# Kernel tuning notes

Hardware: AMD Instinct MI355X
Metric: run time of the kernel (lower is better)

## Reference

```python
import jax, jax.numpy as jnp
import numpy as np

S = 1024      # seq_len (capped by module's precomputed rows/cols tables)
B = 8         # batch
E = 512       # embed_dim
PD = 192      # pos_dim
H = 8         # num_heads
QHD = 32      # query_head_dim (== key_head_dim)
PHD = 4       # pos_head_dim
IN_DIM = (2 * QHD + PHD) * H  # 544


def setup_inputs() -> dict:
    key = jax.random.key(0)
    k0, k1, k2, k3 = jax.random.split(key, 4)
    x = jax.random.normal(k0, (S, B, E), jnp.float32)
    pos_emb = jax.random.normal(k1, (B, 2 * S - 1, PD), jnp.float32)
    # ScaledLinear(embed_dim, in_proj_dim, initial_scale=query_head_dim**-0.25)
    W_in = jax.random.normal(k2, (E, IN_DIM), jnp.float32) * (QHD ** -0.25) / np.sqrt(E).astype(np.float32)
    b_in = jnp.zeros((IN_DIM,), jnp.float32)
    # ScaledLinear(pos_dim, num_heads*pos_head_dim, bias=False, initial_scale=0.05)
    W_pos = jax.random.normal(k3, (PD, H * PHD), jnp.float32) * (0.05 / np.sqrt(PD).astype(np.float32))
    return {"x": x, "pos_emb": pos_emb, "W_in": W_in, "b_in": b_in, "W_pos": W_pos}


def reference(x, pos_emb, W_in, b_in, W_pos):
    s, b, _ = x.shape
    h, qhd, phd = H, QHD, PHD
    qdim = h * qhd

    proj = x @ W_in + b_in                      # [S, B, 544]
    q = proj[..., :qdim].reshape(s, b, h, qhd)          # [S,B,H,Dq]
    k = proj[..., qdim:2 * qdim].reshape(s, b, h, qhd)  # [S,B,H,Dq]
    p = proj[..., 2 * qdim:].reshape(s, b, h, phd)      # [S,B,H,Dp]

    # attn_scores[h,b,i,j] = q_i . k_j
    attn_scores = jnp.einsum('sbhd,tbhd->hbst', q, k)   # [H,B,S,S]

    # positional projection: [B, 2S-1, H, Dp]
    pe = (pos_emb @ W_pos).reshape(b, 2 * s - 1, h, phd)
    pos_scores = jnp.einsum('sbhd,bnhd->hbsn', p, pe)   # [H,B,S,2S-1]

    # relative skew: index[i,j] = (S-1-i) + j  (matches rows[-S:]+cols gather)
    idx = (s - 1) - jnp.arange(s)[:, None] + jnp.arange(s)[None, :]  # [S,S]
    idx_b = jnp.broadcast_to(idx[None, None], (h, b, s, s))
    rel = jnp.take_along_axis(pos_scores, idx_b, axis=-1)            # [H,B,S,S]

    return jax.nn.softmax(attn_scores + rel, axis=-1)
```

## Files before the change

### kernel.cpp

```cpp
#include <hip/hip_runtime.h>
#include <hip/hip_fp16.h>

#define S_LEN 1024
#define BATCH 8
#define EMB 512
#define POSD 192
#define NH 8
#define QHD 32
#define PHD 4
#define IN_DIM 544
#define QDIM 256
#define NPOS 2047

typedef _Float16 half8 __attribute__((ext_vector_type(8)));
typedef _Float16 half4_t __attribute__((ext_vector_type(4)));
typedef _Float16 half2_t __attribute__((ext_vector_type(2)));
typedef float f32x4 __attribute__((ext_vector_type(4)));

static __device__ __forceinline__ float fdot2(half2_t a, half2_t b, float c) {
#if __has_builtin(__builtin_amdgcn_fdot2)
  return __builtin_amdgcn_fdot2(a, b, c, false);
#else
  return c + (float)a[0] * (float)b[0] + (float)a[1] * (float)b[1];
#endif
}

__global__ __launch_bounds__(256) void wconv_kernel(const float* __restrict__ W_in,
                                                    const float* __restrict__ W_pos,
                                                    _Float16* __restrict__ Wt,
                                                    _Float16* __restrict__ WtP) {
  const int blk = blockIdx.x;
  const int tid = threadIdx.x;
  if (blk < 72) {
    __shared__ float T[64][65];
    const int bx = blk % 9;
    const int by = blk / 9;
    const int n0 = bx * 64, e0 = by * 64;
    const int r = tid >> 4, c4 = (tid & 15) * 4;
    if (n0 + c4 < IN_DIM) {
      #pragma unroll
      for (int rr = 0; rr < 64; rr += 16) {
        f32x4 v = *(const f32x4*)(W_in + (size_t)(e0 + r + rr) * IN_DIM + n0 + c4);
        T[r + rr][c4] = v[0]; T[r + rr][c4 + 1] = v[1];
        T[r + rr][c4 + 2] = v[2]; T[r + rr][c4 + 3] = v[3];
      }
    }
    __syncthreads();
    const int nl = tid >> 2, ec = (tid & 3) * 16;
    const int n = n0 + nl;
    if (n < IN_DIM) {
      half8 h0, h1;
      #pragma unroll
      for (int j = 0; j < 8; ++j) {
        h0[j] = (_Float16)T[ec + j][nl];
        h1[j] = (_Float16)T[ec + 8 + j][nl];
      }
      *(half8*)(Wt + (size_t)n * EMB + e0 + ec) = h0;
      *(half8*)(Wt + (size_t)n * EMB + e0 + ec + 8) = h1;
    }
  } else {
    for (int i = tid; i < 32 * POSD; i += 256) {
      int c = i / POSD, k = i % POSD;
      WtP[i] = (_Float16)W_pos[(size_t)k * 32 + c];
    }
  }
}

__global__ __launch_bounds__(256) void pe_kernel(const float* __restrict__ pos_emb,
                                                 const _Float16* __restrict__ WtP,
                                                 _Float16* __restrict__ pe16) {
  __shared__ __align__(16) _Float16 As[64][200];
  const int b = blockIdx.y, chunk = blockIdx.x;
  const int n0 = chunk * 64;
  const int tid = threadIdx.x;
  const int row = tid >> 2, sc = tid & 3;
  const bool rowok = (n0 + row) < NPOS;
  const float* src = pos_emb + ((size_t)b * NPOS + n0 + row) * POSD + sc * 48;
  #pragma unroll
  for (int j = 0; j < 6; ++j) {
    f32x4 v0 = {}, v1 = {};
    if (rowok) { v0 = *(const f32x4*)(src + j * 8); v1 = *(const f32x4*)(src + j * 8 + 4); }
    half8 h;
    #pragma unroll
    for (int t = 0; t < 4; ++t) { h[t] = (_Float16)v0[t]; h[4 + t] = (_Float16)v1[t]; }
    *(half8*)&As[row][sc * 48 + j * 8] = h;
  }
  __syncthreads();
  const int w = tid >> 6, l = tid & 63, g = l >> 4, lg = l & 15;
  f32x4 acc0 = {}, acc1 = {};
  f32x4* accp[2] = {&acc0, &acc1};
  #pragma unroll
  for (int kk = 0; kk < POSD; kk += 32) {
    half8 aF = *(const half8*)&As[w * 16 + lg][kk + g * 8];
    half8 b0 = *(const half8*)(WtP + (size_t)lg * POSD + kk + g * 8);
    half8 b1 = *(const half8*)(WtP + (size_t)(16 + lg) * POSD + kk + g * 8);
    acc0 = __builtin_amdgcn_mfma_f32_16x16x32_f16(aF, b0, acc0, 0, 0, 0);
    acc1 = __builtin_amdgcn_mfma_f32_16x16x32_f16(aF, b1, acc1, 0, 0, 0);
  }
  #pragma unroll
  for (int t = 0; t < 2; ++t) {
    int c = t * 16 + lg, h = c >> 2, d = c & 3;
    _Float16* dst = pe16 + ((size_t)(b * NH + h) * NPOS) * PHD + d;
    f32x4 a = *accp[t];
    #pragma unroll
    for (int r = 0; r < 4; ++r) {
      int n = n0 + w * 16 + 4 * g + r;
      if (n < NPOS) dst[(size_t)n * PHD] = (_Float16)a[r];
    }
  }
}

__global__ __launch_bounds__(256) void proj_kernel(const float* __restrict__ x,
                                                   const _Float16* __restrict__ Wt,
                                                   const float* __restrict__ bias,
                                                   _Float16* __restrict__ q16,
                                                   _Float16* __restrict__ k16,
                                                   _Float16* __restrict__ p16) {
  __shared__ __align__(16) _Float16 As[64][40];
  __shared__ __align__(16) _Float16 Bs[64][40];
  const int m0 = blockIdx.x * 64;
  const int n0 = blockIdx.y * 64;
  const int tid = threadIdx.x;
  const int w = tid >> 6, l = tid & 63, g = l >> 4, lg = l & 15;
  const int wm = w >> 1, wn = w & 1;
  const int srow = tid >> 2, sc = tid & 3;

  f32x4 acc[2][2] = {};

  for (int k0 = 0; k0 < EMB; k0 += 32) {
    const float* asrc = x + (size_t)(m0 + srow) * EMB + k0 + sc * 8;
    f32x4 a0 = *(const f32x4*)asrc;
    f32x4 a1 = *(const f32x4*)(asrc + 4);
    half8 ah;
    #pragma unroll
    for (int j = 0; j < 4; ++j) { ah[j] = (_Float16)a0[j]; ah[4 + j] = (_Float16)a1[j]; }
    int nrow = n0 + srow;
    half8 bh8 = {};
    if (nrow < IN_DIM) bh8 = *(const half8*)(Wt + (size_t)nrow * EMB + k0 + sc * 8);
    *(half8*)&As[srow][sc * 8] = ah;
    *(half8*)&Bs[srow][sc * 8] = bh8;
    __syncthreads();
    half8 aF0 = *(const half8*)&As[wm * 32 + lg][g * 8];
    half8 aF1 = *(const half8*)&As[wm * 32 + 16 + lg][g * 8];
    half8 bF0 = *(const half8*)&Bs[wn * 32 + lg][g * 8];
    half8 bF1 = *(const half8*)&Bs[wn * 32 + 16 + lg][g * 8];
    acc[0][0] = __builtin_amdgcn_mfma_f32_16x16x32_f16(aF0, bF0, acc[0][0], 0, 0, 0);
    acc[0][1] = __builtin_amdgcn_mfma_f32_16x16x32_f16(aF0, bF1, acc[0][1], 0, 0, 0);
    acc[1][0] = __builtin_amdgcn_mfma_f32_16x16x32_f16(aF1, bF0, acc[1][0], 0, 0, 0);
    acc[1][1] = __builtin_amdgcn_mfma_f32_16x16x32_f16(aF1, bF1, acc[1][1], 0, 0, 0);
    __syncthreads();
  }

  #pragma unroll
  for (int sm = 0; sm < 2; ++sm)
    #pragma unroll
    for (int sn = 0; sn < 2; ++sn)
      #pragma unroll
      for (int r = 0; r < 4; ++r) {
        int m = m0 + wm * 32 + sm * 16 + 4 * g + r;
        int n = n0 + wn * 32 + sn * 16 + lg;
        if (n < IN_DIM) {
          float v = acc[sm][sn][r] + bias[n];
          _Float16 hv = (_Float16)v;
          int s = m >> 3, b = m & 7;
          if (n < QDIM) {
            int h = n >> 5, d = n & 31;
            q16[(((size_t)(b * NH + h)) * S_LEN + s) * QHD + d] = hv;
          } else if (n < 2 * QDIM) {
            int n2 = n - QDIM;
            int h = n2 >> 5, d = n2 & 31;
            k16[(((size_t)(b * NH + h)) * S_LEN + s) * QHD + d] = hv;
          } else {
            int n2 = n - 2 * QDIM;
            int h = n2 >> 2, d = n2 & 3;
            p16[(((size_t)(b * NH + h)) * S_LEN + s) * PHD + d] = hv;
          }
        }
      }
}

__global__ __launch_bounds__(256, 4) void attn_kernel(const _Float16* __restrict__ q16,
                                                      const _Float16* __restrict__ k16,
                                                      const _Float16* __restrict__ p16,
                                                      const _Float16* __restrict__ pe16,
                                                      float* __restrict__ out) {
  __shared__ __align__(16) _Float16 peLDS[1040 * 4];
  __shared__ float wred[4][16];
  __shared__ __align__(16) float sbuf[4][16][68];
  const int bid = blockIdx.x;
  const int swz = (bid & 7) * 512 + (bid >> 3);
  const int bh = swz >> 6;
  const int rblk = swz & 63;
  const int b = bh >> 3, h = bh & 7;
  const int i0 = rblk * 16;
  const int tid = threadIdx.x;
  const int w = tid >> 6, l = tid & 63, g = l >> 4, lg = l & 15;
  const int nlo = S_LEN - 16 - i0;

  for (int it = tid; it < 1039; it += 256) {
    *(uint2*)&peLDS[it * 4] =
        *(const uint2*)&pe16[((size_t)bh * NPOS + nlo + it) * 4];
  }

  const _Float16* qbase = q16 + ((size_t)bh * S_LEN + i0) * QHD;
  half8 qF = *(const half8*)(qbase + lg * QHD + g * 8);

  const _Float16* pbase = p16 + ((size_t)bh * S_LEN + i0 + lg) * PHD;
  half2_t pq0 = *(const half2_t*)(pbase);
  half2_t pq1 = *(const half2_t*)(pbase + 2);

  __syncthreads();

  const _Float16* kbase = k16 + (size_t)bh * S_LEN * QHD;
  const int jw = w * 256;
  f32x4 zero = {};
  float s = 0.f;
  half4_t probs[16];

  #pragma unroll
  for (int ct = 0; ct < 16; ++ct) {
    int j = jw + ct * 16 + lg;
    half8 kF = *(const half8*)(kbase + (size_t)j * QHD + g * 8);
    f32x4 a = __builtin_amdgcn_mfma_f32_16x16x32_f16(kF, qF, zero, 0, 0, 0);
    int nl0 = 15 - lg + jw + ct * 16 + 4 * g;
    half4_t ph;
    #pragma unroll
    for (int r = 0; r < 4; ++r) {
      half4_t pv4 = *(const half4_t*)&peLDS[(nl0 + r) * 4];
      half2_t lo = {pv4[0], pv4[1]};
      half2_t hi = {pv4[2], pv4[3]};
      float sc = fdot2(pq1, hi, fdot2(pq0, lo, a[r]));
      float e = __expf(sc - 6.0f);
      s += e;
      ph[r] = (_Float16)e;
    }
    probs[ct] = ph;
  }

  s += __shfl_xor(s, 16);
  s += __shfl_xor(s, 32);
  if (g == 0) wred[w][lg] = s;
  __syncthreads();
  s = (wred[0][lg] + wred[1][lg]) + (wred[2][lg] + wred[3][lg]);
  const float inv = 1.0f / s;

  const size_t orow0 = ((size_t)(h * BATCH + b) * S_LEN + i0) * S_LEN;
  #pragma unroll
  for (int chunk = 0; chunk < 4; ++chunk) {
    #pragma unroll
    for (int cc = 0; cc < 4; ++cc) {
      half4_t ph = probs[chunk * 4 + cc];
      f32x4 v;
      #pragma unroll
      for (int r = 0; r < 4; ++r) v[r] = (float)ph[r] * inv;
      *(f32x4*)&sbuf[w][lg][cc * 16 + 4 * g] = v;
    }
    asm volatile("s_waitcnt lgkmcnt(0)" ::: "memory");
    __builtin_amdgcn_sched_barrier(0);
    #pragma unroll
    for (int k2 = 0; k2 < 4; ++k2) {
      int rr = k2 * 4 + g;
      f32x4 v = *(const f32x4*)&sbuf[w][rr][lg * 4];
      *(f32x4*)(out + orow0 + (size_t)rr * S_LEN + jw + chunk * 64 + lg * 4) = v;
    }
    asm volatile("s_waitcnt lgkmcnt(0)" ::: "memory");
    __builtin_amdgcn_sched_barrier(0);
  }
}

extern "C" void kernel_launch(void* const* d_in, const int* in_sizes, int n_in,
                              void* d_out, int out_size, void* d_ws, size_t ws_size,
                              hipStream_t stream) {
  const float* x = (const float*)d_in[0];
  const float* pos_emb = (const float*)d_in[1];
  const float* W_in = (const float*)d_in[2];
  const float* b_in = (const float*)d_in[3];
  const float* W_pos = (const float*)d_in[4];
  float* out = (float*)d_out;

  char* ws = (char*)d_ws;
  _Float16* Wt = (_Float16*)(ws);
  _Float16* q16 = (_Float16*)(ws + 557056);
  _Float16* k16 = (_Float16*)(ws + 557056 + 4194304);
  _Float16* p16 = (_Float16*)(ws + 557056 + 2 * 4194304);
  _Float16* pe16 = (_Float16*)(ws + 557056 + 2 * 4194304 + 524288);
  _Float16* WtP = p16;

  wconv_kernel<<<dim3(73), dim3(256), 0, stream>>>(W_in, W_pos, Wt, WtP);
  pe_kernel<<<dim3(32, BATCH), dim3(256), 0, stream>>>(pos_emb, WtP, pe16);
  proj_kernel<<<dim3(128, 9), dim3(256), 0, stream>>>(x, Wt, b_in, q16, k16, p16);
  attn_kernel<<<dim3(4096), dim3(256), 0, stream>>>(q16, k16, p16, pe16, out);
}
```

Measured before the change: 91.32 us.

## Merge weight conversion with pos-embedding projection and retile input projection GEMM

Folds the W_pos conversion and the positional projection into one prep kernel. Each block converts W_pos into shared memory itself, so one kernel launch and the global staging buffer go away. The projection GEMM moves to 128x64 tiles with a 64-wide K step, staging fp32 x tiles in swizzled shared memory and converting to fp16 at fragment load. This means fewer barriers and K iterations, at the cost of larger shared memory use and redundant W_pos work in every pe block.

```diff
diff --git a/kernel.cpp b/kernel.cpp
--- a/kernel.cpp
+++ b/kernel.cpp
@@ -25,14 +25,16 @@
 #endif
 }
 
-__global__ __launch_bounds__(256) void wconv_kernel(const float* __restrict__ W_in,
-                                                    const float* __restrict__ W_pos,
-                                                    _Float16* __restrict__ Wt,
-                                                    _Float16* __restrict__ WtP) {
+__global__ __launch_bounds__(256) void prep_kernel(const float* __restrict__ W_in,
+                                                   const float* __restrict__ W_pos,
+                                                   const float* __restrict__ pos_emb,
+                                                   _Float16* __restrict__ Wt,
+                                                   _Float16* __restrict__ pe16) {
+  __shared__ __align__(16) char smem[38400];
   const int blk = blockIdx.x;
   const int tid = threadIdx.x;
   if (blk < 72) {
-    __shared__ float T[64][65];
+    float (*T)[65] = reinterpret_cast<float(*)[65]>(smem);
     const int bx = blk % 9;
     const int by = blk / 9;
     const int n0 = bx * 64, e0 = by * 64;
@@ -59,53 +61,52 @@
       *(half8*)(Wt + (size_t)n * EMB + e0 + ec + 8) = h1;
     }
   } else {
-    for (int i = tid; i < 32 * POSD; i += 256) {
-      int c = i / POSD, k = i % POSD;
-      WtP[i] = (_Float16)W_pos[(size_t)k * 32 + c];
-    }
-  }
-}
-
-__global__ __launch_bounds__(256) void pe_kernel(const float* __restrict__ pos_emb,
-                                                 const _Float16* __restrict__ WtP,
-                                                 _Float16* __restrict__ pe16) {
-  __shared__ __align__(16) _Float16 As[64][200];
-  const int b = blockIdx.y, chunk = blockIdx.x;
-  const int n0 = chunk * 64;
-  const int tid = threadIdx.x;
-  const int row = tid >> 2, sc = tid & 3;
-  const bool rowok = (n0 + row) < NPOS;
-  const float* src = pos_emb + ((size_t)b * NPOS + n0 + row) * POSD + sc * 48;
-  #pragma unroll
-  for (int j = 0; j < 6; ++j) {
-    f32x4 v0 = {}, v1 = {};
-    if (rowok) { v0 = *(const f32x4*)(src + j * 8); v1 = *(const f32x4*)(src + j * 8 + 4); }
-    half8 h;
-    #pragma unroll
-    for (int t = 0; t < 4; ++t) { h[t] = (_Float16)v0[t]; h[4 + t] = (_Float16)v1[t]; }
-    *(half8*)&As[row][sc * 48 + j * 8] = h;
-  }
-  __syncthreads();
-  const int w = tid >> 6, l = tid & 63, g = l >> 4, lg = l & 15;
-  f32x4 acc0 = {}, acc1 = {};
-  f32x4* accp[2] = {&acc0, &acc1};
-  #pragma unroll
-  for (int kk = 0; kk < POSD; kk += 32) {
-    half8 aF = *(const half8*)&As[w * 16 + lg][kk + g * 8];
-    half8 b0 = *(const half8*)(WtP + (size_t)lg * POSD + kk + g * 8);
-    half8 b1 = *(const half8*)(WtP + (size_t)(16 + lg) * POSD + kk + g * 8);
-    acc0 = __builtin_amdgcn_mfma_f32_16x16x32_f16(aF, b0, acc0, 0, 0, 0);
-    acc1 = __builtin_amdgcn_mfma_f32_16x16x32_f16(aF, b1, acc1, 0, 0, 0);
-  }
-  #pragma unroll
-  for (int t = 0; t < 2; ++t) {
-    int c = t * 16 + lg, h = c >> 2, d = c & 3;
-    _Float16* dst = pe16 + ((size_t)(b * NH + h) * NPOS) * PHD + d;
-    f32x4 a = *accp[t];
-    #pragma unroll
-    for (int r = 0; r < 4; ++r) {
-      int n = n0 + w * 16 + 4 * g + r;
-      if (n < NPOS) dst[(size_t)n * PHD] = (_Float16)a[r];
+    _Float16 (*As)[200] = reinterpret_cast<_Float16(*)[200]>(smem);
+    _Float16 (*Wl)[200] = reinterpret_cast<_Float16(*)[200]>(smem + 25600);
+    const int id = blk - 72;
+    const int chunk = id & 31, b = id >> 5;
+    const int n0 = chunk * 64;
+    #pragma unroll
+    for (int p = 0; p < 6; ++p) {
+      int f = (p * 256 + tid) * 4;
+      f32x4 v = *(const f32x4*)(W_pos + f);
+      int k = f >> 5, c = f & 31;
+      #pragma unroll
+      for (int t = 0; t < 4; ++t) Wl[c + t][k] = (_Float16)v[t];
+    }
+    const int row = tid >> 2, sc = tid & 3;
+    const bool rowok = (n0 + row) < NPOS;
+    const float* src = pos_emb + ((size_t)b * NPOS + n0 + row) * POSD + sc * 48;
+    #pragma unroll
+    for (int j = 0; j < 6; ++j) {
+      f32x4 v0 = {}, v1 = {};
+      if (rowok) { v0 = *(const f32x4*)(src + j * 8); v1 = *(const f32x4*)(src + j * 8 + 4); }
+      half8 h;
+      #pragma unroll
+      for (int t = 0; t < 4; ++t) { h[t] = (_Float16)v0[t]; h[4 + t] = (_Float16)v1[t]; }
+      *(half8*)&As[row][sc * 48 + j * 8] = h;
+    }
+    __syncthreads();
+    const int w = tid >> 6, l = tid & 63, g = l >> 4, lg = l & 15;
+    f32x4 acc0 = {}, acc1 = {};
+    #pragma unroll
+    for (int kk = 0; kk < POSD; kk += 32) {
+      half8 aF = *(const half8*)&As[w * 16 + lg][kk + g * 8];
+      half8 b0 = *(const half8*)&Wl[lg][kk + g * 8];
+      half8 b1 = *(const half8*)&Wl[16 + lg][kk + g * 8];
+      acc0 = __builtin_amdgcn_mfma_f32_16x16x32_f16(aF, b0, acc0, 0, 0, 0);
+      acc1 = __builtin_amdgcn_mfma_f32_16x16x32_f16(aF, b1, acc1, 0, 0, 0);
+    }
+    f32x4 accs[2] = {acc0, acc1};
+    #pragma unroll
+    for (int t = 0; t < 2; ++t) {
+      int c = t * 16 + lg, h = c >> 2, d = c & 3;
+      _Float16* dst = pe16 + ((size_t)(b * NH + h) * NPOS) * PHD + d;
+      #pragma unroll
+      for (int r2 = 0; r2 < 4; ++r2) {
+        int n = n0 + w * 16 + 4 * g + r2;
+        if (n < NPOS) dst[(size_t)n * PHD] = (_Float16)accs[t][r2];
+      }
     }
   }
 }
@@ -116,51 +117,73 @@
                                                    _Float16* __restrict__ q16,
                                                    _Float16* __restrict__ k16,
                                                    _Float16* __restrict__ p16) {
-  __shared__ __align__(16) _Float16 As[64][40];
-  __shared__ __align__(16) _Float16 Bs[64][40];
-  const int m0 = blockIdx.x * 64;
+  __shared__ __align__(16) float At[128 * 64];
+  __shared__ __align__(16) _Float16 Bt[64 * 64];
+  const int m0 = blockIdx.x * 128;
   const int n0 = blockIdx.y * 64;
   const int tid = threadIdx.x;
   const int w = tid >> 6, l = tid & 63, g = l >> 4, lg = l & 15;
   const int wm = w >> 1, wn = w & 1;
-  const int srow = tid >> 2, sc = tid & 3;
-
-  f32x4 acc[2][2] = {};
-
-  for (int k0 = 0; k0 < EMB; k0 += 32) {
-    const float* asrc = x + (size_t)(m0 + srow) * EMB + k0 + sc * 8;
-    f32x4 a0 = *(const f32x4*)asrc;
-    f32x4 a1 = *(const f32x4*)(asrc + 4);
-    half8 ah;
-    #pragma unroll
-    for (int j = 0; j < 4; ++j) { ah[j] = (_Float16)a0[j]; ah[4 + j] = (_Float16)a1[j]; }
-    int nrow = n0 + srow;
-    half8 bh8 = {};
-    if (nrow < IN_DIM) bh8 = *(const half8*)(Wt + (size_t)nrow * EMB + k0 + sc * 8);
-    *(half8*)&As[srow][sc * 8] = ah;
-    *(half8*)&Bs[srow][sc * 8] = bh8;
+
+  f32x4 acc[4][2] = {};
+
+  for (int ks = 0; ks < 8; ++ks) {
+    const int k0 = ks * 64;
     __syncthreads();
-    half8 aF0 = *(const half8*)&As[wm * 32 + lg][g * 8];
-    half8 aF1 = *(const half8*)&As[wm * 32 + 16 + lg][g * 8];
-    half8 bF0 = *(const half8*)&Bs[wn * 32 + lg][g * 8];
-    half8 bF1 = *(const half8*)&Bs[wn * 32 + 16 + lg][g * 8];
-    acc[0][0] = __builtin_amdgcn_mfma_f32_16x16x32_f16(aF0, bF0, acc[0][0], 0, 0, 0);
-    acc[0][1] = __builtin_amdgcn_mfma_f32_16x16x32_f16(aF0, bF1, acc[0][1], 0, 0, 0);
-    acc[1][0] = __builtin_amdgcn_mfma_f32_16x16x32_f16(aF1, bF0, acc[1][0], 0, 0, 0);
-    acc[1][1] = __builtin_amdgcn_mfma_f32_16x16x32_f16(aF1, bF1, acc[1][1], 0, 0, 0);
+    #pragma unroll
+    for (int p = 0; p < 8; ++p) {
+      int gl = p * 256 + tid;
+      int r = gl >> 4, j = gl & 15;
+      f32x4 v = *(const f32x4*)(x + (size_t)(m0 + r) * EMB + k0 + j * 4);
+      int jp = (j & 8) | ((j ^ r) & 7);
+      *(f32x4*)((char*)At + r * 256 + jp * 16) = v;
+    }
+    #pragma unroll
+    for (int p = 0; p < 2; ++p) {
+      int gl = p * 256 + tid;
+      int r = gl >> 3, j = gl & 7;
+      half8 v = *(const half8*)(Wt + (size_t)(n0 + r) * EMB + k0 + j * 8);
+      int jp = j ^ (r & 7);
+      *(half8*)((char*)Bt + r * 128 + jp * 16) = v;
+    }
     __syncthreads();
+    #pragma unroll
+    for (int kh = 0; kh < 2; ++kh) {
+      half8 bF[2];
+      #pragma unroll
+      for (int fn = 0; fn < 2; ++fn) {
+        int rB = wn * 32 + fn * 16 + lg;
+        int jB = kh * 4 + g;
+        bF[fn] = *(const half8*)((const char*)Bt + rB * 128 + ((jB ^ (rB & 7)) << 4));
+      }
+      #pragma unroll
+      for (int fm = 0; fm < 4; ++fm) {
+        int rA = wm * 64 + fm * 16 + lg;
+        int j0 = kh * 8 + g * 2;
+        f32x4 lo = *(const f32x4*)((const char*)At + rA * 256 +
+                                   (((j0 & 8) | ((j0 ^ rA) & 7)) << 4));
+        int j1 = j0 + 1;
+        f32x4 hi = *(const f32x4*)((const char*)At + rA * 256 +
+                                   (((j1 & 8) | ((j1 ^ rA) & 7)) << 4));
+        half8 aF;
+        #pragma unroll
+        for (int t = 0; t < 4; ++t) { aF[t] = (_Float16)lo[t]; aF[4 + t] = (_Float16)hi[t]; }
+        acc[fm][0] = __builtin_amdgcn_mfma_f32_16x16x32_f16(aF, bF[0], acc[fm][0], 0, 0, 0);
+        acc[fm][1] = __builtin_amdgcn_mfma_f32_16x16x32_f16(aF, bF[1], acc[fm][1], 0, 0, 0);
+      }
+    }
   }
 
   #pragma unroll
-  for (int sm = 0; sm < 2; ++sm)
-    #pragma unroll
-    for (int sn = 0; sn < 2; ++sn)
+  for (int fm = 0; fm < 4; ++fm)
+    #pragma unroll
+    for (int fn = 0; fn < 2; ++fn)
       #pragma unroll
       for (int r = 0; r < 4; ++r) {
-        int m = m0 + wm * 32 + sm * 16 + 4 * g + r;
-        int n = n0 + wn * 32 + sn * 16 + lg;
+        int m = m0 + wm * 64 + fm * 16 + 4 * g + r;
+        int n = n0 + wn * 32 + fn * 16 + lg;
         if (n < IN_DIM) {
-          float v = acc[sm][sn][r] + bias[n];
+          float v = acc[fm][fn][r] + bias[n];
           _Float16 hv = (_Float16)v;
           int s = m >> 3, b = m & 7;
           if (n < QDIM) {
@@ -284,10 +307,8 @@
   _Float16* k16 = (_Float16*)(ws + 557056 + 4194304);
   _Float16* p16 = (_Float16*)(ws + 557056 + 2 * 4194304);
   _Float16* pe16 = (_Float16*)(ws + 557056 + 2 * 4194304 + 524288);
-  _Float16* WtP = p16;
-
-  wconv_kernel<<<dim3(73), dim3(256), 0, stream>>>(W_in, W_pos, Wt, WtP);
-  pe_kernel<<<dim3(32, BATCH), dim3(256), 0, stream>>>(pos_emb, WtP, pe16);
-  proj_kernel<<<dim3(128, 9), dim3(256), 0, stream>>>(x, Wt, b_in, q16, k16, p16);
+
+  prep_kernel<<<dim3(328), dim3(256), 0, stream>>>(W_in, W_pos, pos_emb, Wt, pe16);
+  proj_kernel<<<dim3(64, 9), dim3(256), 0, stream>>>(x, Wt, b_in, q16, k16, p16);
   attn_kernel<<<dim3(4096), dim3(256), 0, stream>>>(q16, k16, p16, pe16, out);
 }
```

Measured after the change: 112.9 us. 23.7% more time.
